# Kernel tuning notes

Hardware: AMD Instinct MI355X
Metric: run time of the kernel (lower is better)

Reference implementation:

```python
import jax, jax.numpy as jnp
import numpy as np

BS, N, FEAT = 4, 4096, 64
LN_EPS = 1e-5


def setup_inputs() -> dict:
    key = jax.random.key(0)
    k1, k2, k3 = jax.random.split(key, 3)
    positions = jax.random.normal(k1, (BS, N, 3), dtype=jnp.float32)
    # nn.Linear(n_point, feature_dim): weight (FEAT, N), bias (FEAT,)
    W = jax.random.normal(k2, (FEAT, N), dtype=jnp.float32) * (1.0 / np.sqrt(N))
    b = jax.random.normal(k3, (FEAT,), dtype=jnp.float32) * 0.02
    gamma = jnp.ones((FEAT,), dtype=jnp.float32)
    beta = jnp.zeros((FEAT,), dtype=jnp.float32)
    return {"positions": positions, "W": W, "b": b, "gamma": gamma, "beta": beta}


def reference(positions, W, b, gamma, beta):
    # all-pairs squared distances: (bs, N, N)
    diff = positions[:, :, None, :] - positions[:, None, :, :]  # (bs,N,N,3)
    sq = jnp.sum(diff * diff, axis=-1)                          # (bs,N,N)
    # safe sqrt (diagonal is exactly 0)
    safe = jnp.where(sq > 0, sq, 1.0)
    dist = jnp.where(sq > 0, jnp.sqrt(safe), 0.0)               # (bs,N,N)
    # Linear(N -> FEAT)
    x = jnp.einsum('bnm,fm->bnf', dist, W) + b                  # (bs,N,FEAT)
    # LayerNorm over last dim (biased variance, eps=1e-5)
    mu = jnp.mean(x, axis=-1, keepdims=True)
    var = jnp.mean((x - mu) ** 2, axis=-1, keepdims=True)
    xn = (x - mu) / jnp.sqrt(var + LN_EPS) * gamma + beta
    # SiLU
    return xn * jax.nn.sigmoid(xn)
```

## Files before the change

### kernel.cpp

```cpp
#include <hip/hip_runtime.h>


typedef float f32x4 __attribute__((ext_vector_type(4)));
typedef __bf16 bf16x8 __attribute__((ext_vector_type(8)));

union BF8 { bf16x8 v; uint4 u; };

#define N_PTS 4096
#define FEATD 64
#define BK 256
#define NCH (N_PTS / BK)

__global__ void wconv_kernel(const float* __restrict__ W,
                             unsigned short* __restrict__ Wbt) {
  int gid = blockIdx.x * blockDim.x + threadIdx.x;
  int f = gid >> 9, m8 = gid & 511;
  const float4* src = (const float4*)(W + (size_t)f * N_PTS + m8 * 8);
  float4 a = src[0], b = src[1];
  BF8 o;
  o.v[0] = (__bf16)a.x; o.v[1] = (__bf16)a.y; o.v[2] = (__bf16)a.z; o.v[3] = (__bf16)a.w;
  o.v[4] = (__bf16)b.x; o.v[5] = (__bf16)b.y; o.v[6] = (__bf16)b.z; o.v[7] = (__bf16)b.w;
  ((uint4*)Wbt)[(size_t)m8 * 64 + f] = o.u;
}

__device__ __forceinline__ void load_lds16(const void* g, void* l) {
  __builtin_amdgcn_global_load_lds(
      (const __attribute__((address_space(1))) void*)g,
      (__attribute__((address_space(3))) void*)l, 16, 0, 0);
}

__global__ __launch_bounds__(1024, 4) void frp_kernel(
    const float* __restrict__ pos, const float* __restrict__ W,
    const float* __restrict__ bias, const float* __restrict__ gamma,
    const float* __restrict__ beta, const unsigned short* __restrict__ Wbt,
    float* __restrict__ out) {
  __shared__ uint4 Wbuf[2][2048];
  __shared__ __align__(16) float Px[N_PTS];
  __shared__ __align__(16) float Py[N_PTS];
  __shared__ __align__(16) float Pz[N_PTS];

  const int tid = threadIdx.x;
  const int lane = tid & 63;
  const int wave = tid >> 6;
  const int rs  = wave & 1;
  const int ksl = wave >> 1;
  const int fx = lane & 15;
  const int q = lane >> 4;

  const int batch = blockIdx.x >> 6;
  const int nb = (blockIdx.x & 63) * 64;
  const float* posB = pos + (size_t)batch * N_PTS * 3;

  {
    const float4* p4 = (const float4*)posB;
    float4 f0 = p4[tid * 3 + 0];
    float4 f1 = p4[tid * 3 + 1];
    float4 f2 = p4[tid * 3 + 2];
    ((float4*)Px)[tid] = make_float4(f0.x, f0.w, f1.z, f2.y);
    ((float4*)Py)[tid] = make_float4(f0.y, f1.x, f1.w, f2.z);
    ((float4*)Pz)[tid] = make_float4(f0.z, f1.y, f2.x, f2.w);
  }

  const bool useWb = (Wbt != nullptr);

  auto stageW = [&](int c, int b) {
#pragma unroll
    for (int it = 0; it < 2; ++it) {
      int gi = it * 1024 + tid;
      if (useWb) {
        load_lds16(Wbt + ((size_t)c * 2048 + gi) * 8, &Wbuf[b][gi]);
      } else {
        int g = gi >> 6, f = gi & 63;
        const float4* src = (const float4*)(W + (size_t)f * N_PTS + c * BK + g * 8);
        float4 a = src[0], b2 = src[1];
        BF8 o;
        o.v[0] = (__bf16)a.x;  o.v[1] = (__bf16)a.y;  o.v[2] = (__bf16)a.z;  o.v[3] = (__bf16)a.w;
        o.v[4] = (__bf16)b2.x; o.v[5] = (__bf16)b2.y; o.v[6] = (__bf16)b2.z; o.v[7] = (__bf16)b2.w;
        Wbuf[b][gi] = o.u;
      }
    }
  };

  f32x4 acc[2][4];
#pragma unroll
  for (int a = 0; a < 2; ++a)
#pragma unroll
    for (int t = 0; t < 4; ++t) acc[a][t] = (f32x4){0.f, 0.f, 0.f, 0.f};

  stageW(0, 0);
  __syncthreads();

  const int nrow0 = nb + rs * 32 + fx;
  const float px0 = Px[nrow0],      py0 = Py[nrow0],      pz0 = Pz[nrow0];
  const float px1 = Px[nrow0 + 16], py1 = Py[nrow0 + 16], pz1 = Pz[nrow0 + 16];

  const int g8 = ksl * 4 + q;

  for (int c = 0; c < NCH; ++c) {
    if (c + 1 < NCH) stageW(c + 1, (c + 1) & 1);
    const uint4* Wcur = Wbuf[c & 1];
    const int m4 = c * 64 + g8 * 2;
    f32x4 xa = ((const f32x4*)Px)[m4], xb = ((const f32x4*)Px)[m4 + 1];
    f32x4 ya = ((const f32x4*)Py)[m4], yb = ((const f32x4*)Py)[m4 + 1];
    f32x4 za = ((const f32x4*)Pz)[m4], zb = ((const f32x4*)Pz)[m4 + 1];

    bf16x8 af0, af1;
    {
      f32x4 dx = xa - px0, dy = ya - py0, dz = za - pz0;
      f32x4 sq = dx * dx + dy * dy + dz * dz;
#pragma unroll
      for (int j = 0; j < 4; ++j) af0[j] = (__bf16)__builtin_amdgcn_sqrtf(sq[j]);
      dx = xb - px0; dy = yb - py0; dz = zb - pz0;
      sq = dx * dx + dy * dy + dz * dz;
#pragma unroll
      for (int j = 0; j < 4; ++j) af0[4 + j] = (__bf16)__builtin_amdgcn_sqrtf(sq[j]);
      dx = xa - px1; dy = ya - py1; dz = za - pz1;
      sq = dx * dx + dy * dy + dz * dz;
#pragma unroll
      for (int j = 0; j < 4; ++j) af1[j] = (__bf16)__builtin_amdgcn_sqrtf(sq[j]);
      dx = xb - px1; dy = yb - py1; dz = zb - pz1;
      sq = dx * dx + dy * dy + dz * dz;
#pragma unroll
      for (int j = 0; j < 4; ++j) af1[4 + j] = (__bf16)__builtin_amdgcn_sqrtf(sq[j]);
    }
#pragma unroll
    for (int t = 0; t < 4; ++t) {
      BF8 bw;
      bw.u = Wcur[g8 * 64 + t * 16 + fx];
      acc[0][t] = __builtin_amdgcn_mfma_f32_16x16x32_bf16(af0, bw.v, acc[0][t], 0, 0, 0);
      acc[1][t] = __builtin_amdgcn_mfma_f32_16x16x32_bf16(af1, bw.v, acc[1][t], 0, 0, 0);
    }
    __syncthreads();
  }

  f32x4* mbv = (f32x4*)Wbuf;
  __syncthreads();
  if (ksl >= 4) {
    int w = (ksl - 4) * 2 + rs;
#pragma unroll
    for (int a = 0; a < 2; ++a)
#pragma unroll
      for (int t = 0; t < 4; ++t)
        mbv[w * 512 + (a * 4 + t) * 64 + lane] = acc[a][t];
  }
  __syncthreads();
  if (ksl < 4) {
    int w = ksl * 2 + rs;
#pragma unroll
    for (int a = 0; a < 2; ++a)
#pragma unroll
      for (int t = 0; t < 4; ++t)
        acc[a][t] += mbv[w * 512 + (a * 4 + t) * 64 + lane];
  }
  __syncthreads();
  if (ksl >= 1 && ksl < 4) {
    int w = (ksl - 1) * 2 + rs;
#pragma unroll
    for (int a = 0; a < 2; ++a)
#pragma unroll
      for (int t = 0; t < 4; ++t)
        mbv[w * 512 + (a * 4 + t) * 64 + lane] = acc[a][t];
  }
  __syncthreads();
  if (ksl == 0) {
#pragma unroll
    for (int s = 0; s < 3; ++s)
#pragma unroll
      for (int a = 0; a < 2; ++a)
#pragma unroll
        for (int t = 0; t < 4; ++t)
          acc[a][t] += mbv[(s * 2 + rs) * 512 + (a * 4 + t) * 64 + lane];

    float bb[4], gg[4], be[4];
#pragma unroll
    for (int t = 0; t < 4; ++t) {
      bb[t] = bias[t * 16 + fx];
      gg[t] = gamma[t * 16 + fx];
      be[t] = beta[t * 16 + fx];
    }
    float* outB = out + ((size_t)batch * N_PTS + nb + rs * 32) * FEATD;
#pragma unroll
    for (int a = 0; a < 2; ++a) {
#pragma unroll
      for (int r = 0; r < 4; ++r) {
        float x[4], d[4];
#pragma unroll
        for (int t = 0; t < 4; ++t) x[t] = acc[a][t][r] + bb[t];
        float s = x[0] + x[1] + x[2] + x[3];
        s += __shfl_xor(s, 1); s += __shfl_xor(s, 2);
        s += __shfl_xor(s, 4); s += __shfl_xor(s, 8);
        float mu = s * (1.f / 64.f);
        float v = 0.f;
#pragma unroll
        for (int t = 0; t < 4; ++t) { d[t] = x[t] - mu; v += d[t] * d[t]; }
        v += __shfl_xor(v, 1); v += __shfl_xor(v, 2);
        v += __shfl_xor(v, 4); v += __shfl_xor(v, 8);
        float rstd = __builtin_amdgcn_rsqf(v * (1.f / 64.f) + 1e-5f);
        float* orow = outB + (a * 16 + q * 4 + r) * FEATD;
#pragma unroll
        for (int t = 0; t < 4; ++t) {
          float xn = d[t] * rstd * gg[t] + be[t];
          float y = xn * (1.f / (1.f + __expf(-xn)));
          orow[t * 16 + fx] = y;
        }
      }
    }
  }
}

extern "C" void kernel_launch(void* const* d_in, const int* in_sizes, int n_in,
                              void* d_out, int out_size, void* d_ws, size_t ws_size,
                              hipStream_t stream) {
  const float* pos   = (const float*)d_in[0];
  const float* W     = (const float*)d_in[1];
  const float* bias  = (const float*)d_in[2];
  const float* gamma = (const float*)d_in[3];
  const float* beta  = (const float*)d_in[4];
  float* out = (float*)d_out;

  const size_t wb_bytes = (size_t)FEATD * N_PTS * sizeof(unsigned short);
  int use_ws = (d_ws != nullptr && ws_size >= wb_bytes);
  unsigned short* Wbt = use_ws ? (unsigned short*)d_ws : nullptr;

  if (use_ws) {
    wconv_kernel<<<dim3((FEATD * N_PTS / 8) / 256), dim3(256), 0, stream>>>(W, Wbt);
  }
  frp_kernel<<<dim3(256), dim3(1024), 0, stream>>>(pos, W, bias, gamma, beta, Wbt, out);
}
```

Before: 86.86 us.

## Give each wave a private W buffer and drop per-chunk block barriers

Replaces the block-shared double-buffered W tile with a per-wave private LDS slot. Each wave stages only the W slices it consumes and synchronizes with explicit waitcnts instead of a __syncthreads every K chunk. The next chunk's load is issued right after the current fragments are read into registers. This removes block-wide barrier stalls and lets waves drift independently. In exchange, waves that share the same ksl now fetch the same W data twice, and each load is exposed only for the MFMA and distance phase.

```diff
diff --git a/kernel.cpp b/kernel.cpp
--- a/kernel.cpp
+++ b/kernel.cpp
@@ -34,7 +34,7 @@
     const float* __restrict__ bias, const float* __restrict__ gamma,
     const float* __restrict__ beta, const unsigned short* __restrict__ Wbt,
     float* __restrict__ out) {
-  __shared__ uint4 Wbuf[2][2048];
+  __shared__ uint4 Wpriv[16][256];
   __shared__ __align__(16) float Px[N_PTS];
   __shared__ __align__(16) float Py[N_PTS];
   __shared__ __align__(16) float Pz[N_PTS];
@@ -63,20 +63,22 @@
 
   const bool useWb = (Wbt != nullptr);
 
-  auto stageW = [&](int c, int b) {
-#pragma unroll
-    for (int it = 0; it < 2; ++it) {
-      int gi = it * 1024 + tid;
-      if (useWb) {
-        load_lds16(Wbt + ((size_t)c * 2048 + gi) * 8, &Wbuf[b][gi]);
-      } else {
-        int g = gi >> 6, f = gi & 63;
-        const float4* src = (const float4*)(W + (size_t)f * N_PTS + c * BK + g * 8);
-        float4 a = src[0], b2 = src[1];
+  auto stageW = [&](int c) {
+    if (useWb) {
+#pragma unroll
+      for (int i = 0; i < 4; ++i)
+        load_lds16(Wbt + ((size_t)((c * 32 + ksl * 4 + i) * 64 + lane)) * 8,
+                   &Wpriv[wave][i * 64 + lane]);
+    } else {
+#pragma unroll
+      for (int i = 0; i < 4; ++i) {
+        const float4* src =
+            (const float4*)(W + (size_t)lane * N_PTS + c * BK + (ksl * 4 + i) * 8);
+        float4 a4 = src[0], b4 = src[1];
         BF8 o;
-        o.v[0] = (__bf16)a.x;  o.v[1] = (__bf16)a.y;  o.v[2] = (__bf16)a.z;  o.v[3] = (__bf16)a.w;
-        o.v[4] = (__bf16)b2.x; o.v[5] = (__bf16)b2.y; o.v[6] = (__bf16)b2.z; o.v[7] = (__bf16)b2.w;
-        Wbuf[b][gi] = o.u;
+        o.v[0] = (__bf16)a4.x; o.v[1] = (__bf16)a4.y; o.v[2] = (__bf16)a4.z; o.v[3] = (__bf16)a4.w;
+        o.v[4] = (__bf16)b4.x; o.v[5] = (__bf16)b4.y; o.v[6] = (__bf16)b4.z; o.v[7] = (__bf16)b4.w;
+        Wpriv[wave][i * 64 + lane] = o.u;
       }
     }
   };
@@ -87,7 +89,7 @@
 #pragma unroll
     for (int t = 0; t < 4; ++t) acc[a][t] = (f32x4){0.f, 0.f, 0.f, 0.f};
 
-  stageW(0, 0);
+  stageW(0);
   __syncthreads();
 
   const int nrow0 = nb + rs * 32 + fx;
@@ -97,8 +99,6 @@
   const int g8 = ksl * 4 + q;
 
   for (int c = 0; c < NCH; ++c) {
-    if (c + 1 < NCH) stageW(c + 1, (c + 1) & 1);
-    const uint4* Wcur = Wbuf[c & 1];
     const int m4 = c * 64 + g8 * 2;
     f32x4 xa = ((const f32x4*)Px)[m4], xb = ((const f32x4*)Px)[m4 + 1];
     f32x4 ya = ((const f32x4*)Py)[m4], yb = ((const f32x4*)Py)[m4 + 1];
@@ -123,17 +123,28 @@
 #pragma unroll
       for (int j = 0; j < 4; ++j) af1[4 + j] = (__bf16)__builtin_amdgcn_sqrtf(sq[j]);
     }
+
+    if (useWb) asm volatile("s_waitcnt vmcnt(0)" ::: "memory");
+    __builtin_amdgcn_sched_barrier(0);
+
+    BF8 bw[4];
+#pragma unroll
+    for (int t = 0; t < 4; ++t)
+      bw[t].u = Wpriv[wave][q * 64 + t * 16 + fx];
+    asm volatile("s_waitcnt lgkmcnt(0)" ::: "memory");
+    __builtin_amdgcn_sched_barrier(0);
+
+    if (c + 1 < NCH) stageW(c + 1);
+    __builtin_amdgcn_sched_barrier(0);
+
 #pragma unroll
     for (int t = 0; t < 4; ++t) {
-      BF8 bw;
-      bw.u = Wcur[g8 * 64 + t * 16 + fx];
-      acc[0][t] = __builtin_amdgcn_mfma_f32_16x16x32_bf16(af0, bw.v, acc[0][t], 0, 0, 0);
-      acc[1][t] = __builtin_amdgcn_mfma_f32_16x16x32_bf16(af1, bw.v, acc[1][t], 0, 0, 0);
-    }
-    __syncthreads();
-  }
-
-  f32x4* mbv = (f32x4*)Wbuf;
+      acc[0][t] = __builtin_amdgcn_mfma_f32_16x16x32_bf16(af0, bw[t].v, acc[0][t], 0, 0, 0);
+      acc[1][t] = __builtin_amdgcn_mfma_f32_16x16x32_bf16(af1, bw[t].v, acc[1][t], 0, 0, 0);
+    }
+  }
+
+  f32x4* mbv = (f32x4*)Wpriv;
   __syncthreads();
   if (ksl >= 4) {
     int w = (ksl - 4) * 2 + rs;
```

After: 90.69 us. +4.4%, slower.

## Load W fragments directly from global into registers, dropping LDS staging and per-chunk barriers

Applied to the files above, without the earlier changes.

Removes the double-buffered LDS staging of the bf16 weight chunk and the __syncthreads per K-chunk. Each lane now prefetches its own four W fragments for the next chunk from global/L2 into registers, one iteration ahead. The position loads are also split into two halves to lower register pressure, and the loop is unrolled by 2. This drops barrier stalls and LDS traffic, but every wave now reads W from global memory separately, which adds L2 traffic and exposes load latency.

```diff
diff --git a/kernel.cpp b/kernel.cpp
--- a/kernel.cpp
+++ b/kernel.cpp
@@ -23,21 +23,15 @@
   ((uint4*)Wbt)[(size_t)m8 * 64 + f] = o.u;
 }
 
-__device__ __forceinline__ void load_lds16(const void* g, void* l) {
-  __builtin_amdgcn_global_load_lds(
-      (const __attribute__((address_space(1))) void*)g,
-      (__attribute__((address_space(3))) void*)l, 16, 0, 0);
-}
-
 __global__ __launch_bounds__(1024, 4) void frp_kernel(
     const float* __restrict__ pos, const float* __restrict__ W,
     const float* __restrict__ bias, const float* __restrict__ gamma,
     const float* __restrict__ beta, const unsigned short* __restrict__ Wbt,
     float* __restrict__ out) {
-  __shared__ uint4 Wbuf[2][2048];
   __shared__ __align__(16) float Px[N_PTS];
   __shared__ __align__(16) float Py[N_PTS];
   __shared__ __align__(16) float Pz[N_PTS];
+  __shared__ f32x4 mbv[4096];
 
   const int tid = threadIdx.x;
   const int lane = tid & 63;
@@ -62,24 +56,8 @@
   }
 
   const bool useWb = (Wbt != nullptr);
-
-  auto stageW = [&](int c, int b) {
-#pragma unroll
-    for (int it = 0; it < 2; ++it) {
-      int gi = it * 1024 + tid;
-      if (useWb) {
-        load_lds16(Wbt + ((size_t)c * 2048 + gi) * 8, &Wbuf[b][gi]);
-      } else {
-        int g = gi >> 6, f = gi & 63;
-        const float4* src = (const float4*)(W + (size_t)f * N_PTS + c * BK + g * 8);
-        float4 a = src[0], b2 = src[1];
-        BF8 o;
-        o.v[0] = (__bf16)a.x;  o.v[1] = (__bf16)a.y;  o.v[2] = (__bf16)a.z;  o.v[3] = (__bf16)a.w;
-        o.v[4] = (__bf16)b2.x; o.v[5] = (__bf16)b2.y; o.v[6] = (__bf16)b2.z; o.v[7] = (__bf16)b2.w;
-        Wbuf[b][gi] = o.u;
-      }
-    }
-  };
+  const uint4* Wg = (const uint4*)Wbt;
+  const int g8 = ksl * 4 + q;
 
   f32x4 acc[2][4];
 #pragma unroll
@@ -87,53 +65,81 @@
 #pragma unroll
     for (int t = 0; t < 4; ++t) acc[a][t] = (f32x4){0.f, 0.f, 0.f, 0.f};
 
-  stageW(0, 0);
+  uint4 bwc[4];
+  if (useWb) {
+#pragma unroll
+    for (int t = 0; t < 4; ++t) bwc[t] = Wg[g8 * 64 + t * 16 + fx];
+  }
+
   __syncthreads();
 
   const int nrow0 = nb + rs * 32 + fx;
   const float px0 = Px[nrow0],      py0 = Py[nrow0],      pz0 = Pz[nrow0];
   const float px1 = Px[nrow0 + 16], py1 = Py[nrow0 + 16], pz1 = Pz[nrow0 + 16];
 
-  const int g8 = ksl * 4 + q;
-
+#pragma unroll 2
   for (int c = 0; c < NCH; ++c) {
-    if (c + 1 < NCH) stageW(c + 1, (c + 1) & 1);
-    const uint4* Wcur = Wbuf[c & 1];
+    uint4 bwn[4];
+    if (useWb) {
+      const int Gn = (((c + 1) & (NCH - 1)) * 32 + g8) * 64;
+#pragma unroll
+      for (int t = 0; t < 4; ++t) bwn[t] = Wg[Gn + t * 16 + fx];
+    }
+
     const int m4 = c * 64 + g8 * 2;
-    f32x4 xa = ((const f32x4*)Px)[m4], xb = ((const f32x4*)Px)[m4 + 1];
-    f32x4 ya = ((const f32x4*)Py)[m4], yb = ((const f32x4*)Py)[m4 + 1];
-    f32x4 za = ((const f32x4*)Pz)[m4], zb = ((const f32x4*)Pz)[m4 + 1];
-
     bf16x8 af0, af1;
     {
+      f32x4 xa = ((const f32x4*)Px)[m4];
+      f32x4 ya = ((const f32x4*)Py)[m4];
+      f32x4 za = ((const f32x4*)Pz)[m4];
       f32x4 dx = xa - px0, dy = ya - py0, dz = za - pz0;
       f32x4 sq = dx * dx + dy * dy + dz * dz;
 #pragma unroll
       for (int j = 0; j < 4; ++j) af0[j] = (__bf16)__builtin_amdgcn_sqrtf(sq[j]);
-      dx = xb - px0; dy = yb - py0; dz = zb - pz0;
-      sq = dx * dx + dy * dy + dz * dz;
-#pragma unroll
-      for (int j = 0; j < 4; ++j) af0[4 + j] = (__bf16)__builtin_amdgcn_sqrtf(sq[j]);
       dx = xa - px1; dy = ya - py1; dz = za - pz1;
       sq = dx * dx + dy * dy + dz * dz;
 #pragma unroll
       for (int j = 0; j < 4; ++j) af1[j] = (__bf16)__builtin_amdgcn_sqrtf(sq[j]);
+    }
+    {
+      f32x4 xb = ((const f32x4*)Px)[m4 + 1];
+      f32x4 yb = ((const f32x4*)Py)[m4 + 1];
+      f32x4 zb = ((const f32x4*)Pz)[m4 + 1];
+      f32x4 dx = xb - px0, dy = yb - py0, dz = zb - pz0;
+      f32x4 sq = dx * dx + dy * dy + dz * dz;
+#pragma unroll
+      for (int j = 0; j < 4; ++j) af0[4 + j] = (__bf16)__builtin_amdgcn_sqrtf(sq[j]);
       dx = xb - px1; dy = yb - py1; dz = zb - pz1;
       sq = dx * dx + dy * dy + dz * dz;
 #pragma unroll
       for (int j = 0; j < 4; ++j) af1[4 + j] = (__bf16)__builtin_amdgcn_sqrtf(sq[j]);
     }
-#pragma unroll
-    for (int t = 0; t < 4; ++t) {
-      BF8 bw;
-      bw.u = Wcur[g8 * 64 + t * 16 + fx];
-      acc[0][t] = __builtin_amdgcn_mfma_f32_16x16x32_bf16(af0, bw.v, acc[0][t], 0, 0, 0);
-      acc[1][t] = __builtin_amdgcn_mfma_f32_16x16x32_bf16(af1, bw.v, acc[1][t], 0, 0, 0);
-    }
-    __syncthreads();
-  }
-
-  f32x4* mbv = (f32x4*)Wbuf;
+
+    if (useWb) {
+#pragma unroll
+      for (int t = 0; t < 4; ++t) {
+        BF8 bw;
+        bw.u = bwc[t];
+        acc[0][t] = __builtin_amdgcn_mfma_f32_16x16x32_bf16(af0, bw.v, acc[0][t], 0, 0, 0);
+        acc[1][t] = __builtin_amdgcn_mfma_f32_16x16x32_bf16(af1, bw.v, acc[1][t], 0, 0, 0);
+      }
+#pragma unroll
+      for (int t = 0; t < 4; ++t) bwc[t] = bwn[t];
+    } else {
+#pragma unroll
+      for (int t = 0; t < 4; ++t) {
+        const int G = c * 32 + g8;
+        const float4* src = (const float4*)(W + (size_t)(t * 16 + fx) * N_PTS + G * 8);
+        float4 a4 = src[0], b4 = src[1];
+        BF8 bw;
+        bw.v[0] = (__bf16)a4.x; bw.v[1] = (__bf16)a4.y; bw.v[2] = (__bf16)a4.z; bw.v[3] = (__bf16)a4.w;
+        bw.v[4] = (__bf16)b4.x; bw.v[5] = (__bf16)b4.y; bw.v[6] = (__bf16)b4.z; bw.v[7] = (__bf16)b4.w;
+        acc[0][t] = __builtin_amdgcn_mfma_f32_16x16x32_bf16(af0, bw.v, acc[0][t], 0, 0, 0);
+        acc[1][t] = __builtin_amdgcn_mfma_f32_16x16x32_bf16(af1, bw.v, acc[1][t], 0, 0, 0);
+      }
+    }
+  }
+
   __syncthreads();
   if (ksl >= 4) {
     int w = (ksl - 4) * 2 + rs;
```

Measured after the change: 159.9 us. 84.0% more time.
